# Optimization experiments

Measured on AMD Instinct MI355X. Metric: run time of the kernel, lower is better.

## Reference

```python
import jax, jax.numpy as jnp
import numpy as np

N_NODES = 100000
N_EDGES = 3200000
D_FEAT = 128


def setup_inputs() -> dict:
    key = jax.random.key(0)
    k1, k2, k3, k4 = jax.random.split(key, 4)
    edge_row = jax.random.randint(k1, (N_EDGES,), 0, N_NODES, dtype=jnp.int64 if jax.config.jax_enable_x64 else jnp.int32)
    edge_col = jax.random.randint(k2, (N_EDGES,), 0, N_NODES, dtype=edge_row.dtype)
    edge_val = jax.random.uniform(k3, (N_EDGES,), dtype=jnp.float32)
    embeds = jax.random.normal(k4, (N_NODES, D_FEAT), dtype=jnp.float32)
    return {"edge_row": edge_row, "edge_col": edge_col, "edge_val": edge_val, "embeds": embeds}


def reference(edge_row, edge_col, edge_val, embeds):
    # SpMM: out[r] = sum_{e: row(e)=r} val(e) * embeds[col(e)]
    messages = edge_val[:, None] * embeds[edge_col]  # [E, D]
    out = jax.ops.segment_sum(messages, edge_row, num_segments=embeds.shape[0])  # [N, D]
    return out
```

## Files before the change

kernel.cpp:

```cpp
#include <hip/hip_runtime.h>
#include <hip/hip_bf16.h>
#include <stdint.h>

#define N_NODES 100000
#define D_FEAT  128
#define RSH     5
#define RPB     32
#define NBUCK   ((N_NODES + RPB - 1) / RPB)
#define CAPF    1152
#define KMAX    ((CAPF + 255) / 256)
#define OCAP    8192
#define SC_THR  1024
#define SC_EPT  16
#define SC_TILE (SC_THR * SC_EPT)
#define COLMASK 0x1FFFF

__global__ __launch_bounds__(256) void conv_bf16_kernel(const float2* __restrict__ in,
                                                        uint32_t* __restrict__ outp, int n2) {
    int i = blockIdx.x * 256 + threadIdx.x;
    if (i < n2) {
        float2 f = in[i];
        uint32_t bx = __float_as_uint(f.x); bx = (bx + 0x7FFFu + ((bx >> 16) & 1u)) >> 16;
        uint32_t by = __float_as_uint(f.y); by = (by + 0x7FFFu + ((by >> 16) & 1u)) >> 16;
        outp[i] = bx | (by << 16);
    }
}

__global__ __launch_bounds__(SC_THR) void scatter_fixed_kernel(
    const int* __restrict__ row, const int* __restrict__ col,
    const float* __restrict__ val, int* __restrict__ cursor,
    int2* __restrict__ rec, int4* __restrict__ oflow, int* __restrict__ ocnt, int n)
{
    __shared__ int cnt[NBUCK];
    __shared__ int base[NBUCK];
    const int tid = threadIdx.x;
    const int e0  = blockIdx.x * SC_TILE + tid * SC_EPT;

    for (int i = tid; i < NBUCK; i += SC_THR) cnt[i] = 0;
    __syncthreads();

    int   r[SC_EPT], c[SC_EPT];
    float v[SC_EPT];
    if (e0 + SC_EPT <= n) {
        const int4* rp = (const int4*)(row + e0);
        const int4* cp = (const int4*)(col + e0);
        const float4* vp = (const float4*)(val + e0);
        #pragma unroll
        for (int q = 0; q < SC_EPT / 4; q++) {
            int4 rr = rp[q]; int4 cc = cp[q]; float4 vv = vp[q];
            r[q*4+0]=rr.x; r[q*4+1]=rr.y; r[q*4+2]=rr.z; r[q*4+3]=rr.w;
            c[q*4+0]=cc.x; c[q*4+1]=cc.y; c[q*4+2]=cc.z; c[q*4+3]=cc.w;
            v[q*4+0]=vv.x; v[q*4+1]=vv.y; v[q*4+2]=vv.z; v[q*4+3]=vv.w;
        }
    } else {
        #pragma unroll
        for (int k = 0; k < SC_EPT; k++) {
            int e = e0 + k;
            if (e < n) { r[k] = row[e]; c[k] = col[e]; v[k] = val[e]; }
            else       { r[k] = -1; }
        }
    }

    int rk[SC_EPT];
    #pragma unroll
    for (int k = 0; k < SC_EPT; k++)
        if (r[k] >= 0) rk[k] = atomicAdd(&cnt[r[k] >> RSH], 1);
    __syncthreads();

    for (int i = tid; i < NBUCK; i += SC_THR) {
        int cc = cnt[i];
        if (cc) base[i] = atomicAdd(&cursor[i], cc);
    }
    __syncthreads();

    #pragma unroll
    for (int k = 0; k < SC_EPT; k++) {
        if (r[k] >= 0) {
            int bk  = r[k] >> RSH;
            int pos = base[bk] + rk[k];
            if (pos < CAPF) {
                rec[(size_t)bk * CAPF + pos] =
                    make_int2(((r[k] & (RPB - 1)) << 17) | c[k], __float_as_int(v[k]));
            } else {
                int op = atomicAdd(ocnt, 1);
                if (op < OCAP) oflow[op] = make_int4(r[k], c[k], __float_as_int(v[k]), 0);
            }
        }
    }
}

template <bool BF16>
__global__ __launch_bounds__(256) void spmm_fixed_kernel(const int* __restrict__ fill,
                                                         const int2* __restrict__ rec,
                                                         const void* __restrict__ emb,
                                                         float* __restrict__ out)
{
    __shared__ int2 buf[CAPF];
    __shared__ int  cnt[RPB];
    __shared__ int  start[RPB];
    __shared__ int  sc_[RPB];

    const int tid  = threadIdx.x;
    const int lane = tid & 63;
    const int wv   = tid >> 6;
    const int b    = blockIdx.x;
    const int m    = min(fill[b], CAPF);
    const size_t beg = (size_t)b * CAPF;
    const uint32_t* __restrict__ embu = (const uint32_t*)emb;
    const float2*   __restrict__ emb2 = (const float2*)emb;

    if (tid < RPB) cnt[tid] = 0;
    __syncthreads();

    int2 rc[KMAX];
    int  rk[KMAX];
    #pragma unroll
    for (int k = 0; k < KMAX; k++) {
        int i = k * 256 + tid;
        if (i < m) {
            rc[k] = rec[beg + i];
            rk[k] = atomicAdd(&cnt[rc[k].x >> 17], 1);
        }
    }
    __syncthreads();
    if (tid < RPB) sc_[tid] = cnt[tid];
    __syncthreads();
    for (int off = 1; off < RPB; off <<= 1) {
        int t = 0;
        if (tid < RPB && tid >= off) t = sc_[tid - off];
        __syncthreads();
        if (tid < RPB) sc_[tid] += t;
        __syncthreads();
    }
    if (tid < RPB) start[tid] = sc_[tid] - cnt[tid];
    __syncthreads();
    #pragma unroll
    for (int k = 0; k < KMAX; k++) {
        int i = k * 256 + tid;
        if (i < m) buf[start[rc[k].x >> 17] + rk[k]] = rc[k];
    }
    __syncthreads();

    for (int rl = wv * 8; rl < wv * 8 + 8; rl++) {
        const int s0 = start[rl];
        const int c0 = cnt[rl];
        float ax = 0.f, ay = 0.f;
        int j = 0;
        for (; j + 8 <= c0; j += 8) {
            int2 e[8];
            #pragma unroll
            for (int q = 0; q < 8; q++) e[q] = buf[s0 + j + q];
            float mx[8], my[8], vv[8];
            #pragma unroll
            for (int q = 0; q < 8; q++) {
                int cc = e[q].x & COLMASK;
                vv[q] = __int_as_float(e[q].y);
                if (BF16) {
                    uint32_t u = embu[(size_t)cc * 64 + lane];
                    mx[q] = __uint_as_float(u << 16);
                    my[q] = __uint_as_float(u & 0xFFFF0000u);
                } else {
                    float2 mm = emb2[(size_t)cc * 64 + lane];
                    mx[q] = mm.x; my[q] = mm.y;
                }
            }
            #pragma unroll
            for (int q = 0; q < 8; q++) { ax += vv[q] * mx[q]; ay += vv[q] * my[q]; }
        }
        for (; j < c0; j++) {
            int2 e = buf[s0 + j];
            int cc = e.x & COLMASK;
            float vv = __int_as_float(e.y);
            float mx, my;
            if (BF16) {
                uint32_t u = embu[(size_t)cc * 64 + lane];
                mx = __uint_as_float(u << 16);
                my = __uint_as_float(u & 0xFFFF0000u);
            } else {
                float2 mm = emb2[(size_t)cc * 64 + lane];
                mx = mm.x; my = mm.y;
            }
            ax += vv * mx; ay += vv * my;
        }
        float2* o = (float2*)(out + (size_t)(b * RPB + rl) * D_FEAT);
        o[lane] = make_float2(ax, ay);
    }
}

__global__ __launch_bounds__(256) void oflow_kernel(const int4* __restrict__ oflow,
                                                    const int* __restrict__ ocnt,
                                                    const float* __restrict__ embeds,
                                                    float* __restrict__ out) {
    const int nof  = min(*ocnt, OCAP);
    const int lane = threadIdx.x & 63;
    const int w    = (blockIdx.x * 256 + threadIdx.x) >> 6;
    const int nw   = (gridDim.x * 256) >> 6;
    for (int i = w; i < nof; i += nw) {
        int4 e = oflow[i];
        const float2* src = (const float2*)(embeds + (size_t)e.y * D_FEAT);
        float2 mm = src[lane];
        float vv = __int_as_float(e.z);
        float* dst = out + (size_t)e.x * D_FEAT + (lane << 1);
        unsafeAtomicAdd(dst,     vv * mm.x);
        unsafeAtomicAdd(dst + 1, vv * mm.y);
    }
}

__global__ __launch_bounds__(256) void spmm_atomic_kernel(
    const int* __restrict__ edge_row, const int* __restrict__ edge_col,
    const float* __restrict__ edge_val, const float* __restrict__ embeds,
    float* __restrict__ out, int n_edges)
{
    const int lane    = threadIdx.x & 63;
    const int wave_id = (blockIdx.x * blockDim.x + threadIdx.x) >> 6;
    const int n_waves = (gridDim.x * blockDim.x) >> 6;
    for (int e = wave_id; e < n_edges; e += n_waves) {
        const int   r = edge_row[e];
        const int   c = edge_col[e];
        const float vv = edge_val[e];
        const float2* src = (const float2*)(embeds + (size_t)c * D_FEAT);
        float2 mm = src[lane];
        float* dst = out + (size_t)r * D_FEAT + (lane << 1);
        unsafeAtomicAdd(dst,     vv * mm.x);
        unsafeAtomicAdd(dst + 1, vv * mm.y);
    }
}

static inline size_t align256(size_t x) { return (x + 255) & ~(size_t)255; }

extern "C" void kernel_launch(void* const* d_in, const int* in_sizes, int n_in,
                              void* d_out, int out_size, void* d_ws, size_t ws_size,
                              hipStream_t stream) {
    const int*   edge_row = (const int*)d_in[0];
    const int*   edge_col = (const int*)d_in[1];
    const float* edge_val = (const float*)d_in[2];
    const float* embeds   = (const float*)d_in[3];
    float*       out      = (float*)d_out;

    const int n_edges = in_sizes[0];

    size_t off = 0;
    size_t o_cursor = off; off = align256(off + (size_t)(NBUCK + 1) * 4);
    size_t o_oflow  = off; off = align256(off + (size_t)OCAP * 16);
    size_t o_rec    = off; off = align256(off + (size_t)NBUCK * CAPF * 8);
    const size_t need_fp32 = off;
    size_t o_emb    = off; off = align256(off + (size_t)N_NODES * 64 * 4);
    const size_t need_bf16 = off;

    if (ws_size < need_fp32) {
        hipMemsetAsync(out, 0, (size_t)out_size * sizeof(float), stream);
        spmm_atomic_kernel<<<dim3(4096), dim3(256), 0, stream>>>(
            edge_row, edge_col, edge_val, embeds, out, n_edges);
        return;
    }

    char* ws = (char*)d_ws;
    int*      cursor = (int*)(ws + o_cursor);
    int*      ocnt   = cursor + NBUCK;
    int4*     oflow  = (int4*)(ws + o_oflow);
    int2*     rec    = (int2*)(ws + o_rec);
    uint32_t* embbf  = (uint32_t*)(ws + o_emb);

    const bool use_bf16 = (ws_size >= need_bf16);

    hipMemsetAsync(cursor, 0, (size_t)(NBUCK + 1) * 4, stream);
    if (use_bf16) {
        const int n2 = N_NODES * (D_FEAT / 2);
        conv_bf16_kernel<<<dim3((n2 + 255) / 256), dim3(256), 0, stream>>>(
            (const float2*)embeds, embbf, n2);
    }
    scatter_fixed_kernel<<<dim3((n_edges + SC_TILE - 1) / SC_TILE), dim3(SC_THR), 0, stream>>>(
        edge_row, edge_col, edge_val, cursor, rec, oflow, ocnt, n_edges);
    if (use_bf16)
        spmm_fixed_kernel<true><<<dim3(NBUCK), dim3(256), 0, stream>>>(cursor, rec, embbf, out);
    else
        spmm_fixed_kernel<false><<<dim3(NBUCK), dim3(256), 0, stream>>>(cursor, rec, embeds, out);
    oflow_kernel<<<dim3(16), dim3(256), 0, stream>>>(oflow, ocnt, embeds, out);
}
```

Before: 284.7 us.

## Fuse bf16 conversion into scatter, double rows per bucket, deepen gather unroll

Moves the fp32-to-bf16 embedding conversion into the scatter kernel as a grid-stride prologue, which removes one kernel launch. Bucket size grows from 32 to 64 rows, with matching capacity, and scatter edges per thread drop from 16 to 8. The spmm gather now issues 16 loads at a time with a 4-wide remainder loop, uses nontemporal loads and stores, and computes 32-bit offsets. The risks are scatter LDS histogram pressure (NBUCK halves, so LDS use drops), fewer spmm blocks, and heavier conversion work sitting in front of the scatter.

```diff
diff --git a/kernel.cpp b/kernel.cpp
--- a/kernel.cpp
+++ b/kernel.cpp
@@ -1,40 +1,42 @@
 #include <hip/hip_runtime.h>
-#include <hip/hip_bf16.h>
 #include <stdint.h>
 
 #define N_NODES 100000
 #define D_FEAT  128
-#define RSH     5
-#define RPB     32
+#define RSH     6
+#define RPB     64
 #define NBUCK   ((N_NODES + RPB - 1) / RPB)
-#define CAPF    1152
+#define CAPF    2304
 #define KMAX    ((CAPF + 255) / 256)
 #define OCAP    8192
 #define SC_THR  1024
-#define SC_EPT  16
+#define SC_EPT  8
 #define SC_TILE (SC_THR * SC_EPT)
 #define COLMASK 0x1FFFF
-
-__global__ __launch_bounds__(256) void conv_bf16_kernel(const float2* __restrict__ in,
-                                                        uint32_t* __restrict__ outp, int n2) {
-    int i = blockIdx.x * 256 + threadIdx.x;
-    if (i < n2) {
-        float2 f = in[i];
-        uint32_t bx = __float_as_uint(f.x); bx = (bx + 0x7FFFu + ((bx >> 16) & 1u)) >> 16;
-        uint32_t by = __float_as_uint(f.y); by = (by + 0x7FFFu + ((by >> 16) & 1u)) >> 16;
-        outp[i] = bx | (by << 16);
-    }
-}
 
 __global__ __launch_bounds__(SC_THR) void scatter_fixed_kernel(
     const int* __restrict__ row, const int* __restrict__ col,
     const float* __restrict__ val, int* __restrict__ cursor,
-    int2* __restrict__ rec, int4* __restrict__ oflow, int* __restrict__ ocnt, int n)
+    int2* __restrict__ rec, int4* __restrict__ oflow, int* __restrict__ ocnt, int n,
+    const uint64_t* __restrict__ embin, uint32_t* __restrict__ embbf, int do_conv)
 {
     __shared__ int cnt[NBUCK];
     __shared__ int base[NBUCK];
     const int tid = threadIdx.x;
-    const int e0  = blockIdx.x * SC_TILE + tid * SC_EPT;
+
+    if (do_conv) {
+        const int n2 = N_NODES * (D_FEAT / 2);
+        const int stride = (int)gridDim.x * SC_THR;
+        for (int i = (int)blockIdx.x * SC_THR + tid; i < n2; i += stride) {
+            uint64_t u = __builtin_nontemporal_load(embin + i);
+            uint32_t bx = (uint32_t)u, by = (uint32_t)(u >> 32);
+            bx = (bx + 0x7FFFu + ((bx >> 16) & 1u)) >> 16;
+            by = (by + 0x7FFFu + ((by >> 16) & 1u)) >> 16;
+            embbf[i] = bx | (by << 16);
+        }
+    }
+
+    const int e0 = (int)blockIdx.x * SC_TILE + tid * SC_EPT;
 
     for (int i = tid; i < NBUCK; i += SC_THR) cnt[i] = 0;
     __syncthreads();
@@ -105,7 +107,7 @@
     const int wv   = tid >> 6;
     const int b    = blockIdx.x;
     const int m    = min(fill[b], CAPF);
-    const size_t beg = (size_t)b * CAPF;
+    const uint64_t* __restrict__ rec8 = (const uint64_t*)rec + (size_t)b * CAPF;
     const uint32_t* __restrict__ embu = (const uint32_t*)emb;
     const float2*   __restrict__ emb2 = (const float2*)emb;
 
@@ -118,8 +120,10 @@
     for (int k = 0; k < KMAX; k++) {
         int i = k * 256 + tid;
         if (i < m) {
-            rc[k] = rec[beg + i];
-            rk[k] = atomicAdd(&cnt[rc[k].x >> 17], 1);
+            uint64_t u = __builtin_nontemporal_load(rec8 + i);
+            rc[k].x = (int)(uint32_t)u;
+            rc[k].y = (int)(uint32_t)(u >> 32);
+            rk[k] = atomicAdd(&cnt[(uint32_t)rc[k].x >> 17], 1);
         }
     }
     __syncthreads();
@@ -137,53 +141,71 @@
     #pragma unroll
     for (int k = 0; k < KMAX; k++) {
         int i = k * 256 + tid;
-        if (i < m) buf[start[rc[k].x >> 17] + rk[k]] = rc[k];
-    }
-    __syncthreads();
-
-    for (int rl = wv * 8; rl < wv * 8 + 8; rl++) {
+        if (i < m) buf[start[(uint32_t)rc[k].x >> 17] + rk[k]] = rc[k];
+    }
+    __syncthreads();
+
+    for (int rl = wv * 16; rl < wv * 16 + 16; rl++) {
         const int s0 = start[rl];
         const int c0 = cnt[rl];
         float ax = 0.f, ay = 0.f;
         int j = 0;
-        for (; j + 8 <= c0; j += 8) {
-            int2 e[8];
-            #pragma unroll
-            for (int q = 0; q < 8; q++) e[q] = buf[s0 + j + q];
-            float mx[8], my[8], vv[8];
-            #pragma unroll
-            for (int q = 0; q < 8; q++) {
-                int cc = e[q].x & COLMASK;
-                vv[q] = __int_as_float(e[q].y);
+        for (; j + 16 <= c0; j += 16) {
+            uint32_t u[16]; float vv[16]; float2 m2[16];
+            #pragma unroll
+            for (int q = 0; q < 16; q++) {
+                int2 e = buf[s0 + j + q];
+                uint32_t off = (((uint32_t)e.x & COLMASK) << 6) | (uint32_t)lane;
+                vv[q] = __int_as_float(e.y);
+                if (BF16) u[q] = embu[off]; else m2[q] = emb2[off];
+            }
+            #pragma unroll
+            for (int q = 0; q < 16; q++) {
                 if (BF16) {
-                    uint32_t u = embu[(size_t)cc * 64 + lane];
-                    mx[q] = __uint_as_float(u << 16);
-                    my[q] = __uint_as_float(u & 0xFFFF0000u);
+                    ax += vv[q] * __uint_as_float(u[q] << 16);
+                    ay += vv[q] * __uint_as_float(u[q] & 0xFFFF0000u);
                 } else {
-                    float2 mm = emb2[(size_t)cc * 64 + lane];
-                    mx[q] = mm.x; my[q] = mm.y;
+                    ax += vv[q] * m2[q].x; ay += vv[q] * m2[q].y;
                 }
             }
-            #pragma unroll
-            for (int q = 0; q < 8; q++) { ax += vv[q] * mx[q]; ay += vv[q] * my[q]; }
+        }
+        for (; j + 4 <= c0; j += 4) {
+            uint32_t u[4]; float vv[4]; float2 m2[4];
+            #pragma unroll
+            for (int q = 0; q < 4; q++) {
+                int2 e = buf[s0 + j + q];
+                uint32_t off = (((uint32_t)e.x & COLMASK) << 6) | (uint32_t)lane;
+                vv[q] = __int_as_float(e.y);
+                if (BF16) u[q] = embu[off]; else m2[q] = emb2[off];
+            }
+            #pragma unroll
+            for (int q = 0; q < 4; q++) {
+                if (BF16) {
+                    ax += vv[q] * __uint_as_float(u[q] << 16);
+                    ay += vv[q] * __uint_as_float(u[q] & 0xFFFF0000u);
+                } else {
+                    ax += vv[q] * m2[q].x; ay += vv[q] * m2[q].y;
+                }
+            }
         }
         for (; j < c0; j++) {
             int2 e = buf[s0 + j];
-            int cc = e.x & COLMASK;
+            uint32_t off = (((uint32_t)e.x & COLMASK) << 6) | (uint32_t)lane;
             float vv = __int_as_float(e.y);
-            float mx, my;
             if (BF16) {
-                uint32_t u = embu[(size_t)cc * 64 + lane];
-                mx = __uint_as_float(u << 16);
-                my = __uint_as_float(u & 0xFFFF0000u);
+                uint32_t u = embu[off];
+                ax += vv * __uint_as_float(u << 16);
+                ay += vv * __uint_as_float(u & 0xFFFF0000u);
             } else {
-                float2 mm = emb2[(size_t)cc * 64 + lane];
-                mx = mm.x; my = mm.y;
-            }
-            ax += vv * mx; ay += vv * my;
-        }
-        float2* o = (float2*)(out + (size_t)(b * RPB + rl) * D_FEAT);
-        o[lane] = make_float2(ax, ay);
+                float2 mm = emb2[off];
+                ax += vv * mm.x; ay += vv * mm.y;
+            }
+        }
+        const int grow = b * RPB + rl;
+        if (grow < N_NODES) {
+            uint64_t w = (uint64_t)__float_as_uint(ax) | ((uint64_t)__float_as_uint(ay) << 32);
+            __builtin_nontemporal_store(w, (uint64_t*)out + (size_t)grow * 64 + lane);
+        }
     }
 }
 
@@ -193,8 +215,8 @@
                                                     float* __restrict__ out) {
     const int nof  = min(*ocnt, OCAP);
     const int lane = threadIdx.x & 63;
-    const int w    = (blockIdx.x * 256 + threadIdx.x) >> 6;
-    const int nw   = (gridDim.x * 256) >> 6;
+    const int w    = ((int)blockIdx.x * 256 + threadIdx.x) >> 6;
+    const int nw   = ((int)gridDim.x * 256) >> 6;
     for (int i = w; i < nof; i += nw) {
         int4 e = oflow[i];
         const float2* src = (const float2*)(embeds + (size_t)e.y * D_FEAT);
@@ -212,8 +234,8 @@
     float* __restrict__ out, int n_edges)
 {
     const int lane    = threadIdx.x & 63;
-    const int wave_id = (blockIdx.x * blockDim.x + threadIdx.x) >> 6;
-    const int n_waves = (gridDim.x * blockDim.x) >> 6;
+    const int wave_id = ((int)blockIdx.x * blockDim.x + threadIdx.x) >> 6;
+    const int n_waves = ((int)gridDim.x * blockDim.x) >> 6;
     for (int e = wave_id; e < n_edges; e += n_waves) {
         const int   r = edge_row[e];
         const int   c = edge_col[e];
@@ -264,13 +286,9 @@
     const bool use_bf16 = (ws_size >= need_bf16);
 
     hipMemsetAsync(cursor, 0, (size_t)(NBUCK + 1) * 4, stream);
-    if (use_bf16) {
-        const int n2 = N_NODES * (D_FEAT / 2);
-        conv_bf16_kernel<<<dim3((n2 + 255) / 256), dim3(256), 0, stream>>>(
-            (const float2*)embeds, embbf, n2);
-    }
     scatter_fixed_kernel<<<dim3((n_edges + SC_TILE - 1) / SC_TILE), dim3(SC_THR), 0, stream>>>(
-        edge_row, edge_col, edge_val, cursor, rec, oflow, ocnt, n_edges);
+        edge_row, edge_col, edge_val, cursor, rec, oflow, ocnt, n_edges,
+        (const uint64_t*)embeds, embbf, use_bf16 ? 1 : 0);
     if (use_bf16)
         spmm_fixed_kernel<true><<<dim3(NBUCK), dim3(256), 0, stream>>>(cursor, rec, embbf, out);
     else
```

New measurement: 275.4 us. 1.03x faster.
